# Kernel optimization log

Measured on AMD Instinct MI355X. Metric: run time of the kernel, lower is better.

Reference implementation:

```python
import jax, jax.numpy as jnp
from jax import lax
import numpy as np

B, CIN, CP, H, W = 16, 64, 64, 64, 64
K1 = 3   # deformable kernel
K2 = 5   # parallel conv kernel
EPS = 1e-5


def conv2d(x, w, stride, pad):
    return lax.conv_general_dilated(
        x, w, (stride, stride), [(pad, pad), (pad, pad)],
        dimension_numbers=('NCHW', 'OIHW', 'NCHW'))


def batchnorm(x, g, b, m, v):
    scale = g / jnp.sqrt(v + EPS)
    return (x - m[None, :, None, None]) * scale[None, :, None, None] + b[None, :, None, None]


def deform_conv2d(x, offset, weight, stride, pad):
    # x: [B,Cin,H,W], offset: [B,2*K*K,Ho,Wo] (dy,dx interleaved per kernel tap, torchvision layout)
    Bn, Cin, Hn, Wn = x.shape
    Cout, _, K, _ = weight.shape
    KK = K * K
    Ho, Wo = offset.shape[2], offset.shape[3]
    off = offset.reshape(Bn, KK, 2, Ho, Wo)
    dy, dx = off[:, :, 0], off[:, :, 1]                      # [B,KK,Ho,Wo]
    ky, kx = jnp.meshgrid(jnp.arange(K), jnp.arange(K), indexing='ij')
    ky = ky.reshape(KK).astype(x.dtype)
    kx = kx.reshape(KK).astype(x.dtype)
    base_y = (jnp.arange(Ho) * stride - pad).astype(x.dtype)
    base_x = (jnp.arange(Wo) * stride - pad).astype(x.dtype)
    ys = base_y[None, None, :, None] + ky[None, :, None, None] + dy  # [B,KK,Ho,Wo]
    xs = base_x[None, None, None, :] + kx[None, :, None, None] + dx
    y0 = jnp.floor(ys); x0 = jnp.floor(xs)
    wy1 = ys - y0; wx1 = xs - x0
    wy0 = 1.0 - wy1; wx0 = 1.0 - wx1
    flat = x.reshape(Bn, Cin, Hn * Wn)

    def gather(yi, xi):
        valid = ((yi >= 0) & (yi <= Hn - 1) & (xi >= 0) & (xi <= Wn - 1))
        yc = jnp.clip(yi, 0, Hn - 1).astype(jnp.int32)
        xc = jnp.clip(xi, 0, Wn - 1).astype(jnp.int32)
        idx = (yc * Wn + xc).reshape(Bn, -1)                 # [B,KK*Ho*Wo]
        g = jax.vmap(lambda f, i: jnp.take(f, i, axis=1))(flat, idx)
        g = g.reshape(Bn, Cin, KK, Ho, Wo)
        return g * valid.astype(x.dtype)[:, None]

    val = (gather(y0, x0) * (wy0 * wx0)[:, None]
           + gather(y0, x0 + 1) * (wy0 * wx1)[:, None]
           + gather(y0 + 1, x0) * (wy1 * wx0)[:, None]
           + gather(y0 + 1, x0 + 1) * (wy1 * wx1)[:, None])   # [B,Cin,KK,Ho,Wo]
    w_r = weight.reshape(Cout, Cin, KK)
    return jnp.einsum('bcknm,ock->bonm', val, w_r)


def setup_inputs():
    key = jax.random.key(0)
    ks = jax.random.split(key, 18)
    f32 = jnp.float32
    x = jax.random.normal(ks[0], (B, CIN, H, W), f32)
    w_off = jax.random.normal(ks[1], (2 * K1 * K1, CIN, 3, 3), f32) * 0.01
    b_off = jnp.zeros((2 * K1 * K1,), f32)
    w1 = jax.random.normal(ks[2], (CP, CIN, K1, K1), f32) / np.sqrt(CIN * K1 * K1)
    w3 = jax.random.normal(ks[3], (CP, CIN, K2, K2), f32) / np.sqrt(CIN * K2 * K2)
    w2 = jax.random.normal(ks[4], (CP, CP, 3, 3), f32) / np.sqrt(CP * 9)
    def bn(i):
        g = jax.random.uniform(ks[5 + 4 * i], (CP,), f32, 0.5, 1.5)
        b = jax.random.normal(ks[6 + 4 * i], (CP,), f32) * 0.1
        m = jax.random.normal(ks[7 + 4 * i], (CP,), f32) * 0.1
        v = jax.random.uniform(ks[8 + 4 * i], (CP,), f32, 0.5, 1.5)
        return g, b, m, v
    g1, b1, m1, v1 = bn(0)
    g3, b3, m3, v3 = bn(1)
    g2, b2, m2, v2 = bn(2)
    return dict(x=x, w_off=w_off, b_off=b_off, w1=w1, g1=g1, b1=b1, m1=m1, v1=v1,
                w3=w3, g3=g3, b3=b3, m3=m3, v3=v3, w2=w2, g2=g2, b2=b2, m2=m2, v2=v2)


def reference(x, w_off, b_off, w1, g1, b1, m1, v1, w3, g3, b3, m3, v3, w2, g2, b2, m2, v2):
    offset1 = conv2d(x, w_off, 1, 1) + b_off[None, :, None, None]
    out = jax.nn.relu(batchnorm(deform_conv2d(x, offset1, w1, 1, 1), g1, b1, m1, v1))
    out_1 = jax.nn.relu(batchnorm(conv2d(x, w3, 1, 2), g3, b3, m3, v3))
    out = out + out_1
    out = batchnorm(conv2d(out, w2, 1, 1), g2, b2, m2, v2)
    out = out + x  # identity shortcut (stride=1, in_planes==planes)
    return jax.nn.relu(out)
```

## Files before the change

kernel.cpp:

```cpp
#include <hip/hip_runtime.h>
#include <hip/hip_bf16.h>


#define HWv 4096
#define EPSv 1e-5f

typedef __attribute__((ext_vector_type(8))) short bf16x8;
typedef __attribute__((ext_vector_type(16))) float f32x16;
typedef __attribute__((ext_vector_type(2))) float f32x2;

__device__ inline ushort f2bf(float f) {
  __hip_bfloat16 h = __float2bfloat16(f);
  return *(ushort*)&h;
}
__device__ inline float bf2f(ushort u) {
  unsigned int t = ((unsigned int)u) << 16;
  union { unsigned int i; float f; } c; c.i = t; return c.f;
}
__device__ inline float bitsf(unsigned int u) {
  union { unsigned int i; float f; } c; c.i = u; return c.f;
}

__global__ __launch_bounds__(256) void prep_kernel(
    const float* __restrict__ x, const float* __restrict__ w3,
    const float* __restrict__ w2, const float* __restrict__ w1,
    const float* __restrict__ w_off,
    ushort* __restrict__ xT, ushort* __restrict__ w3F,
    ushort* __restrict__ w2F, ushort* __restrict__ w1F,
    ushort* __restrict__ wofF) {
  __shared__ float tile[64][65];
  const int blk = blockIdx.x;
  if (blk < 1024) {
    const int y = blk & 63, b = blk >> 6;
    for (int i = threadIdx.x; i < 4096; i += 256) {
      int ci = i >> 6, xx = i & 63;
      tile[ci][xx] = x[(((size_t)b * 64 + ci) * 64 + y) * 64 + xx];
    }
    __syncthreads();
    for (int i = threadIdx.x; i < 2048; i += 256) {
      int xx = i >> 5, cip = (i & 31) * 2;
      ushort2 v;
      v.x = f2bf(tile[cip][xx]);
      v.y = f2bf(tile[cip + 1][xx]);
      *(ushort2*)&xT[(((size_t)b * 64 + y) * 64 + xx) * 64 + cip] = v;
    }
    return;
  }
  int idx = (blk - 1024) * 256 + threadIdx.x;
  if (idx < 102400) {
    int j = idx & 7, lane = (idx >> 3) & 63, ks = (idx >> 9) & 3;
    int half = (idx >> 11) & 1, kk = idx >> 12;
    int ln = lane & 31, kh = lane >> 5;
    int co = half * 32 + ln, ci = ks * 16 + kh * 8 + j;
    w3F[idx] = f2bf(w3[(co * 64 + ci) * 25 + kk]);
    return;
  }
  idx -= 102400;
  if (idx < 36864) {
    int j = idx & 7, lane = (idx >> 3) & 63, ks = (idx >> 9) & 3;
    int half = (idx >> 11) & 1, kk = idx >> 12;
    int ln = lane & 31, kh = lane >> 5;
    int co = half * 32 + ln, ci = ks * 16 + kh * 8 + j;
    w2F[idx] = f2bf(w2[(co * 64 + ci) * 9 + kk]);
    return;
  }
  idx -= 36864;
  if (idx < 36864) {
    int j = idx & 7, lane = (idx >> 3) & 63, ks = (idx >> 9) & 3;
    int half = (idx >> 11) & 1, kk = idx >> 12;
    int ln = lane & 31, kh = lane >> 5;
    int co = half * 32 + ln, ci = ks * 16 + kh * 8 + j;
    w1F[idx] = f2bf(w1[(co * 64 + ci) * 9 + kk]);
    return;
  }
  idx -= 36864;
  if (idx < 18432) {
    int j = idx & 7, lane = (idx >> 3) & 63, ks = (idx >> 9) & 3;
    int kk = idx >> 11;
    int ln = lane & 31, kh = lane >> 5;
    int ci = ks * 16 + kh * 8 + j;
    wofF[idx] = f2bf(ln < 18 ? w_off[(ln * 64 + ci) * 9 + kk] : 0.f);
  }
}

__device__ __forceinline__ bf16x8 blend4(bf16x8 va, bf16x8 vb, bf16x8 vc, bf16x8 vd,
                                         f32x2 w00v, f32x2 w01v, f32x2 w10v, f32x2 w11v) {
  const unsigned int* ua = (const unsigned int*)&va;
  const unsigned int* ub = (const unsigned int*)&vb;
  const unsigned int* uc = (const unsigned int*)&vc;
  const unsigned int* ud = (const unsigned int*)&vd;
  bf16x8 f;
  ushort2* fo = (ushort2*)&f;
#pragma unroll
  for (int d = 0; d < 4; ++d) {
    f32x2 av = {bitsf(ua[d] << 16), bitsf(ua[d] & 0xFFFF0000u)};
    f32x2 bv = {bitsf(ub[d] << 16), bitsf(ub[d] & 0xFFFF0000u)};
    f32x2 cv = {bitsf(uc[d] << 16), bitsf(uc[d] & 0xFFFF0000u)};
    f32x2 dv = {bitsf(ud[d] << 16), bitsf(ud[d] & 0xFFFF0000u)};
    f32x2 r = w00v * av + w01v * bv + w10v * cv + w11v * dv;
    __hip_bfloat162 h2 = __float22bfloat162_rn(make_float2(r.x, r.y));
    fo[d] = *(ushort2*)&h2;
  }
  return f;
}

__global__ __launch_bounds__(256, 2) void fused_kernel(
    const ushort* __restrict__ xT, const ushort* __restrict__ wofF,
    const float* __restrict__ b_off, const ushort* __restrict__ w1F,
    const ushort* __restrict__ w3F,
    const float* __restrict__ g1, const float* __restrict__ b1,
    const float* __restrict__ m1, const float* __restrict__ v1,
    const float* __restrict__ g3, const float* __restrict__ b3,
    const float* __restrict__ m3, const float* __restrict__ v3,
    ushort* __restrict__ s1T) {
  __shared__ __align__(16) uint4 ldsx[6 * 68 * 8];
  __shared__ float stash[2 * 64 * 18];
  __shared__ float bn1s[64], bn1b[64], bn3s[64], bn3b[64];

  const int tid = threadIdx.x;
  const int wv = tid >> 6, lane = tid & 63;
  const int ln = lane & 31, kh = lane >> 5;
  const int r = wv >> 1, nt = wv & 1;
  const int y0 = blockIdx.x * 2, b = blockIdx.y;
  const int y = y0 + r, px = nt * 32 + ln;
  const uint4* xT4 = (const uint4*)xT;
  const bool interior = (y0 >= 2 && y0 <= 60);

  if (tid < 64) {
    float s = g1[tid] * rsqrtf(v1[tid] + EPSv);
    bn1s[tid] = s; bn1b[tid] = b1[tid] - m1[tid] * s;
    float s3 = g3[tid] * rsqrtf(v3[tid] + EPSv);
    bn3s[tid] = s3; bn3b[tid] = b3[tid] - m3[tid] * s3;
  }
  for (int i = tid; i < 6 * 68 * 8; i += 256) {
    int tr = i / (68 * 8), rem = i % (68 * 8);
    int col = rem >> 3, c = rem & 7;
    int ysrc = min(max(y0 - 2 + tr, 0), 63);
    int xcol = col - 2;
    uint4 v = make_uint4(0, 0, 0, 0);
    if (xcol >= 0 && xcol <= 63)
      v = xT4[((size_t)((b * 64 + ysrc) * 64 + xcol)) * 8 + c];
    ldsx[(tr * 68 + col) * 8 + (c ^ (col & 7))] = v;
  }
  __syncthreads();

  f32x16 acco;
#pragma unroll
  for (int j = 0; j < 16; ++j) acco[j] = 0.f;
  if (interior) {
#pragma unroll
    for (int kk = 0; kk < 9; ++kk) {
      const int ky = kk / 3, kx = kk % 3;
      const int tr = r + ky + 1;
      const int col = px + kx + 1;
      bf16x8 af[4], bf[4];
#pragma unroll
      for (int ks = 0; ks < 4; ++ks)
        af[ks] = *(const bf16x8*)&wofF[(size_t)((kk * 4 + ks) * 64 + lane) * 8];
#pragma unroll
      for (int ks = 0; ks < 4; ++ks) {
        int c = ks * 2 + kh;
        bf[ks] = *(const bf16x8*)&ldsx[(tr * 68 + col) * 8 + (c ^ (col & 7))];
      }
#pragma unroll
      for (int ks = 0; ks < 4; ++ks)
        acco = __builtin_amdgcn_mfma_f32_32x32x16_bf16(af[ks], bf[ks], acco, 0, 0, 0);
    }
  } else {
#pragma unroll
    for (int kk = 0; kk < 9; ++kk) {
      const int ky = kk / 3, kx = kk % 3;
      const int yy = y - 1 + ky;
      if (yy >= 0 && yy <= 63) {
        const int tr = yy - (y0 - 2);
        const int col = px + kx + 1;
#pragma unroll
        for (int ks = 0; ks < 4; ++ks) {
          int c = ks * 2 + kh;
          bf16x8 af = *(const bf16x8*)&wofF[(size_t)((kk * 4 + ks) * 64 + lane) * 8];
          bf16x8 bf = *(const bf16x8*)&ldsx[(tr * 68 + col) * 8 + (c ^ (col & 7))];
          acco = __builtin_amdgcn_mfma_f32_32x32x16_bf16(af, bf, acco, 0, 0, 0);
        }
      }
    }
  }
#pragma unroll
  for (int reg = 0; reg < 16; ++reg) {
    int co = (reg & 3) + 8 * (reg >> 2) + 4 * kh;
    if (co < 18)
      stash[(r * 64 + px) * 18 + co] = acco[reg] + b_off[co];
  }
  __syncthreads();

  float dyv[9], dxv[9];
#pragma unroll
  for (int kk = 0; kk < 9; ++kk) {
    dyv[kk] = stash[(r * 64 + px) * 18 + 2 * kk];
    dxv[kk] = stash[(r * 64 + px) * 18 + 2 * kk + 1];
  }
  bool fast = true;
#pragma unroll
  for (int kk = 0; kk < 9; ++kk) {
    int iy0 = (int)floorf((float)(y - 1 + kk / 3) + dyv[kk]);
    int iy1 = iy0 + 1;
    bool ok0 = (iy0 < 0) || (iy0 > 63) || (iy0 >= y0 - 2 && iy0 <= y0 + 3);
    bool ok1 = (iy1 < 0) || (iy1 > 63) || (iy1 >= y0 - 2 && iy1 <= y0 + 3);
    fast = fast && ok0 && ok1;
  }

  f32x16 accd0, accd1;
#pragma unroll
  for (int j = 0; j < 16; ++j) { accd0[j] = 0.f; accd1[j] = 0.f; }
  const ushort* xb = xT + (size_t)b * 64 * 64 * 64;

  if (__ballot(!fast) == 0ull) {
#pragma unroll
    for (int kk = 0; kk < 9; ++kk) {
      const int ky = kk / 3, kx = kk % 3;
      float ys = (float)(y - 1 + ky) + dyv[kk];
      float xs = (float)(px - 1 + kx) + dxv[kk];
      float y0f = floorf(ys), x0f = floorf(xs);
      float wy1 = ys - y0f, wx1 = xs - x0f;
      float wy0 = 1.f - wy1, wx0 = 1.f - wx1;
      int iy0 = (int)y0f, ix0 = (int)x0f;
      int iy1 = iy0 + 1, ix1 = ix0 + 1;
      float vy0 = (iy0 >= 0 && iy0 <= 63) ? 1.f : 0.f;
      float vy1 = (iy1 >= 0 && iy1 <= 63) ? 1.f : 0.f;
      float vx0 = (ix0 >= 0 && ix0 <= 63) ? 1.f : 0.f;
      float vx1 = (ix1 >= 0 && ix1 <= 63) ? 1.f : 0.f;
      int x0c = min(max(ix0, 0), 63), x1c = min(max(ix1, 0), 63);
      float w00 = wy0 * wx0 * vy0 * vx0;
      float w01 = wy0 * wx1 * vy0 * vx1;
      float w10 = wy1 * wx0 * vy1 * vx0;
      float w11 = wy1 * wx1 * vy1 * vx1;
      int tr0 = min(max(iy0 - (y0 - 2), 0), 5);
      int tr1 = min(max(iy1 - (y0 - 2), 0), 5);
      int c0 = x0c + 2, c1 = x1c + 2;
      f32x2 w00v = {w00, w00}, w01v = {w01, w01};
      f32x2 w10v = {w10, w10}, w11v = {w11, w11};

      bf16x8 a0[4], a1[4], va[4], vb[4], vc[4], vd[4];
#pragma unroll
      for (int ks = 0; ks < 4; ++ks) {
        a0[ks] = *(const bf16x8*)&w1F[(size_t)(((kk * 2 + 0) * 4 + ks) * 64 + lane) * 8];
        a1[ks] = *(const bf16x8*)&w1F[(size_t)(((kk * 2 + 1) * 4 + ks) * 64 + lane) * 8];
      }
#pragma unroll
      for (int ks = 0; ks < 4; ++ks) {
        int c = ks * 2 + kh;
        va[ks] = *(const bf16x8*)&ldsx[(tr0 * 68 + c0) * 8 + (c ^ (c0 & 7))];
        vb[ks] = *(const bf16x8*)&ldsx[(tr0 * 68 + c1) * 8 + (c ^ (c1 & 7))];
        vc[ks] = *(const bf16x8*)&ldsx[(tr1 * 68 + c0) * 8 + (c ^ (c0 & 7))];
        vd[ks] = *(const bf16x8*)&ldsx[(tr1 * 68 + c1) * 8 + (c ^ (c1 & 7))];
      }
#pragma unroll
      for (int ks = 0; ks < 4; ++ks) {
        bf16x8 f = blend4(va[ks], vb[ks], vc[ks], vd[ks], w00v, w01v, w10v, w11v);
        accd0 = __builtin_amdgcn_mfma_f32_32x32x16_bf16(a0[ks], f, accd0, 0, 0, 0);
        accd1 = __builtin_amdgcn_mfma_f32_32x32x16_bf16(a1[ks], f, accd1, 0, 0, 0);
      }
    }
  } else {
#pragma unroll
    for (int kk = 0; kk < 9; ++kk) {
      const int ky = kk / 3, kx = kk % 3;
      float ys = (float)(y - 1 + ky) + dyv[kk];
      float xs = (float)(px - 1 + kx) + dxv[kk];
      float y0f = floorf(ys), x0f = floorf(xs);
      float wy1 = ys - y0f, wx1 = xs - x0f;
      float wy0 = 1.f - wy1, wx0 = 1.f - wx1;
      int iy0 = (int)y0f, ix0 = (int)x0f;
      int iy1 = iy0 + 1, ix1 = ix0 + 1;
      float vy0 = (iy0 >= 0 && iy0 <= 63) ? 1.f : 0.f;
      float vy1 = (iy1 >= 0 && iy1 <= 63) ? 1.f : 0.f;
      float vx0 = (ix0 >= 0 && ix0 <= 63) ? 1.f : 0.f;
      float vx1 = (ix1 >= 0 && ix1 <= 63) ? 1.f : 0.f;
      int x0c = min(max(ix0, 0), 63), x1c = min(max(ix1, 0), 63);
      float w00 = wy0 * wx0 * vy0 * vx0;
      float w01 = wy0 * wx1 * vy0 * vx1;
      float w10 = wy1 * wx0 * vy1 * vx0;
      float w11 = wy1 * wx1 * vy1 * vx1;
      int tr0 = min(max(iy0 - (y0 - 2), 0), 5);
      int tr1 = min(max(iy1 - (y0 - 2), 0), 5);
      int c0 = x0c + 2, c1 = x1c + 2;
      f32x2 w00v = {w00, w00}, w01v = {w01, w01};
      f32x2 w10v = {w10, w10}, w11v = {w11, w11};

      bf16x8 frag[4];
#pragma unroll
      for (int ks = 0; ks < 4; ++ks) {
        int c = ks * 2 + kh;
        bf16x8 va = *(const bf16x8*)&ldsx[(tr0 * 68 + c0) * 8 + (c ^ (c0 & 7))];
        bf16x8 vb = *(const bf16x8*)&ldsx[(tr0 * 68 + c1) * 8 + (c ^ (c1 & 7))];
        bf16x8 vc = *(const bf16x8*)&ldsx[(tr1 * 68 + c0) * 8 + (c ^ (c0 & 7))];
        bf16x8 vd = *(const bf16x8*)&ldsx[(tr1 * 68 + c1) * 8 + (c ^ (c1 & 7))];
        frag[ks] = blend4(va, vb, vc, vd, w00v, w01v, w10v, w11v);
      }
      if (!fast) {
        int y0c = min(max(iy0, 0), 63), y1c = min(max(iy1, 0), 63);
        const ushort* p00 = xb + (y0c * 64 + x0c) * 64 + kh * 8;
        const ushort* p01 = xb + (y0c * 64 + x1c) * 64 + kh * 8;
        const ushort* p10 = xb + (y1c * 64 + x0c) * 64 + kh * 8;
        const ushort* p11 = xb + (y1c * 64 + x1c) * 64 + kh * 8;
#pragma unroll
        for (int ks = 0; ks < 4; ++ks) {
          bf16x8 va = *(const bf16x8*)(p00 + ks * 16);
          bf16x8 vb = *(const bf16x8*)(p01 + ks * 16);
          bf16x8 vc = *(const bf16x8*)(p10 + ks * 16);
          bf16x8 vd = *(const bf16x8*)(p11 + ks * 16);
          frag[ks] = blend4(va, vb, vc, vd, w00v, w01v, w10v, w11v);
        }
      }
#pragma unroll
      for (int ks = 0; ks < 4; ++ks) {
        bf16x8 a0 = *(const bf16x8*)&w1F[(size_t)(((kk * 2 + 0) * 4 + ks) * 64 + lane) * 8];
        bf16x8 a1 = *(const bf16x8*)&w1F[(size_t)(((kk * 2 + 1) * 4 + ks) * 64 + lane) * 8];
        accd0 = __builtin_amdgcn_mfma_f32_32x32x16_bf16(a0, frag[ks], accd0, 0, 0, 0);
        accd1 = __builtin_amdgcn_mfma_f32_32x32x16_bf16(a1, frag[ks], accd1, 0, 0, 0);
      }
    }
  }

  f32x16 acc50, acc51;
#pragma unroll
  for (int j = 0; j < 16; ++j) { acc50[j] = 0.f; acc51[j] = 0.f; }
  if (interior) {
#pragma unroll
    for (int kk = 0; kk < 25; ++kk) {
      const int ky = kk / 5, kx = kk % 5;
      const int tr = r + ky;
      const int col = px + kx;
      bf16x8 a0[4], a1[4], bfv[4];
#pragma unroll
      for (int ks = 0; ks < 4; ++ks) {
        a0[ks] = *(const bf16x8*)&w3F[(size_t)(((kk * 2 + 0) * 4 + ks) * 64 + lane) * 8];
        a1[ks] = *(const bf16x8*)&w3F[(size_t)(((kk * 2 + 1) * 4 + ks) * 64 + lane) * 8];
      }
#pragma unroll
      for (int ks = 0; ks < 4; ++ks) {
        int c = ks * 2 + kh;
        bfv[ks] = *(const bf16x8*)&ldsx[(tr * 68 + col) * 8 + (c ^ (col & 7))];
      }
#pragma unroll
      for (int ks = 0; ks < 4; ++ks) {
        acc50 = __builtin_amdgcn_mfma_f32_32x32x16_bf16(a0[ks], bfv[ks], acc50, 0, 0, 0);
        acc51 = __builtin_amdgcn_mfma_f32_32x32x16_bf16(a1[ks], bfv[ks], acc51, 0, 0, 0);
      }
    }
  } else {
#pragma unroll
    for (int kk = 0; kk < 25; ++kk) {
      const int ky = kk / 5, kx = kk % 5;
      const int yy = y - 2 + ky;
      if (yy >= 0 && yy <= 63) {
        const int tr = r + ky;
        const int col = px + kx;
#pragma unroll
        for (int ks = 0; ks < 4; ++ks) {
          int c = ks * 2 + kh;
          bf16x8 bf = *(const bf16x8*)&ldsx[(tr * 68 + col) * 8 + (c ^ (col & 7))];
          bf16x8 a0 = *(const bf16x8*)&w3F[(size_t)(((kk * 2 + 0) * 4 + ks) * 64 + lane) * 8];
          bf16x8 a1 = *(const bf16x8*)&w3F[(size_t)(((kk * 2 + 1) * 4 + ks) * 64 + lane) * 8];
          acc50 = __builtin_amdgcn_mfma_f32_32x32x16_bf16(a0, bf, acc50, 0, 0, 0);
          acc51 = __builtin_amdgcn_mfma_f32_32x32x16_bf16(a1, bf, acc51, 0, 0, 0);
        }
      }
    }
  }

  ushort* op = s1T + ((size_t)((b * 64 + y) * 64 + px)) * 64;
#pragma unroll
  for (int q = 0; q < 4; ++q) {
    int co0 = 8 * q + 4 * kh;
    float vv[4];
#pragma unroll
    for (int rr = 0; rr < 4; ++rr) {
      int co = co0 + rr;
      float vd = accd0[q * 4 + rr] * bn1s[co] + bn1b[co];
      vd = vd > 0.f ? vd : 0.f;
      float v5 = acc50[q * 4 + rr] * bn3s[co] + bn3b[co];
      v5 = v5 > 0.f ? v5 : 0.f;
      vv[rr] = vd + v5;
    }
    ushort4 st;
    st.x = f2bf(vv[0]); st.y = f2bf(vv[1]); st.z = f2bf(vv[2]); st.w = f2bf(vv[3]);
    *(ushort4*)(op + co0) = st;
#pragma unroll
    for (int rr = 0; rr < 4; ++rr) {
      int co = co0 + 32 + rr;
      float vd = accd1[q * 4 + rr] * bn1s[co] + bn1b[co];
      vd = vd > 0.f ? vd : 0.f;
      float v5 = acc51[q * 4 + rr] * bn3s[co] + bn3b[co];
      v5 = v5 > 0.f ? v5 : 0.f;
      vv[rr] = vd + v5;
    }
    st.x = f2bf(vv[0]); st.y = f2bf(vv[1]); st.z = f2bf(vv[2]); st.w = f2bf(vv[3]);
    *(ushort4*)(op + co0 + 32) = st;
  }
}

__global__ __launch_bounds__(256, 2) void conv3_mfma_kernel(
    const ushort* __restrict__ s1T, const ushort* __restrict__ w2F,
    const float* __restrict__ g2, const float* __restrict__ b2,
    const float* __restrict__ m2, const float* __restrict__ v2,
    const float* __restrict__ x, float* __restrict__ out) {
  __shared__ __align__(16) uint4 Bt[3 * 66 * 8];
  __shared__ float sc[64], bi[64];
  const int tid = threadIdx.x;
  if (tid < 64) {
    float s = g2[tid] * rsqrtf(v2[tid] + EPSv);
    sc[tid] = s;
    bi[tid] = b2[tid] - m2[tid] * s;
  }
  const int y = blockIdx.x, b = blockIdx.y;
  const int wv = tid >> 6, lane = tid & 63;
  const int ln = lane & 31, kh = lane >> 5;
  const int mh = wv & 1, nt = wv >> 1;
  const int px = nt * 32 + ln;
  const uint4* s1T4 = (const uint4*)s1T;

  for (int i = tid; i < 3 * 66 * 8; i += 256) {
    int tr = i / (66 * 8), rem = i % (66 * 8);
    int col = rem >> 3, c = rem & 7;
    int yy = y - 1 + tr, xcol = col - 1;
    uint4 v = make_uint4(0, 0, 0, 0);
    if (yy >= 0 && yy <= 63 && xcol >= 0 && xcol <= 63)
      v = s1T4[((size_t)((b * 64 + yy) * 64 + xcol)) * 8 + c];
    Bt[(tr * 66 + col) * 8 + (c ^ (col & 7))] = v;
  }
  __syncthreads();

  f32x16 acc;
#pragma unroll
  for (int j = 0; j < 16; ++j) acc[j] = 0.f;

#pragma unroll
  for (int kk = 0; kk < 9; ++kk) {
    const int ky = kk / 3, kx = kk % 3;
    const int col = px + kx;
    bf16x8 af[4], bfr[4];
#pragma unroll
    for (int ccb = 0; ccb < 4; ++ccb)
      af[ccb] = *(const bf16x8*)&w2F[(size_t)(((kk * 2 + mh) * 4 + ccb) * 64 + lane) * 8];
#pragma unroll
    for (int ccb = 0; ccb < 4; ++ccb) {
      int c = ccb * 2 + kh;
      bfr[ccb] = *(const bf16x8*)&Bt[(ky * 66 + col) * 8 + (c ^ (col & 7))];
    }
#pragma unroll
    for (int ccb = 0; ccb < 4; ++ccb)
      acc = __builtin_amdgcn_mfma_f32_32x32x16_bf16(af[ccb], bfr[ccb], acc, 0, 0, 0);
  }
#pragma unroll
  for (int reg = 0; reg < 16; ++reg) {
    int co = (reg & 3) + 8 * (reg >> 2) + 4 * kh + mh * 32;
    size_t o = (((size_t)b * 64 + co) * 64 + y) * 64 + px;
    float v = acc[reg] * sc[co] + bi[co] + x[o];
    out[o] = v > 0.f ? v : 0.f;
  }
}

extern "C" void kernel_launch(void* const* d_in, const int* in_sizes, int n_in,
                              void* d_out, int out_size, void* d_ws, size_t ws_size,
                              hipStream_t stream) {
  const float* x     = (const float*)d_in[0];
  const float* w_off = (const float*)d_in[1];
  const float* b_off = (const float*)d_in[2];
  const float* w1    = (const float*)d_in[3];
  const float* g1    = (const float*)d_in[4];
  const float* b1    = (const float*)d_in[5];
  const float* m1    = (const float*)d_in[6];
  const float* v1    = (const float*)d_in[7];
  const float* w3    = (const float*)d_in[8];
  const float* g3    = (const float*)d_in[9];
  const float* b3    = (const float*)d_in[10];
  const float* m3    = (const float*)d_in[11];
  const float* v3    = (const float*)d_in[12];
  const float* w2    = (const float*)d_in[13];
  const float* g2    = (const float*)d_in[14];
  const float* b2    = (const float*)d_in[15];
  const float* m2    = (const float*)d_in[16];
  const float* v2    = (const float*)d_in[17];
  float* out = (float*)d_out;

  ushort* xT   = (ushort*)d_ws;
  ushort* s1T  = xT + (size_t)16 * 64 * HWv;
  ushort* w3F  = s1T + (size_t)16 * 64 * HWv;
  ushort* w2F  = w3F + 102400;
  ushort* w1F  = w2F + 36864;
  ushort* wofF = w1F + 36864;

  prep_kernel<<<dim3(1024 + 760), dim3(256), 0, stream>>>(x, w3, w2, w1, w_off,
                                                          xT, w3F, w2F, w1F, wofF);
  fused_kernel<<<dim3(32, 16), dim3(256), 0, stream>>>(xT, wofF, b_off, w1F, w3F,
                                                       g1, b1, m1, v1, g3, b3, m3, v3,
                                                       s1T);
  conv3_mfma_kernel<<<dim3(64, 16), dim3(256), 0, stream>>>(s1T, w2F, g2, b2, m2, v2,
                                                            x, out);
}
```

Baseline: 69.00 us.

## Split fused kernel K-dimension across two wave halves with LDS reduction

Doubles the fused kernel's block to 512 threads and splits each MFMA reduction over input channels into two halves, one per wave group. Partial offset-conv results are summed through two LDS stash buffers, and the deform and 5x5 accumulators are reduced through a swizzled LDS exchange before the BN/ReLU epilogue. The aim is more waves per CU to hide LDS and gather latency, since the grid has only 512 blocks. The cost is extra barriers, LDS traffic for the reductions, a larger LDS footprint, and half the waves idling during the epilogue.

```diff
diff --git a/kernel.cpp b/kernel.cpp
--- a/kernel.cpp
+++ b/kernel.cpp
@@ -104,7 +104,7 @@
   return f;
 }
 
-__global__ __launch_bounds__(256, 2) void fused_kernel(
+__global__ __launch_bounds__(512, 4) void fused_kernel(
     const ushort* __restrict__ xT, const ushort* __restrict__ wofF,
     const float* __restrict__ b_off, const ushort* __restrict__ w1F,
     const ushort* __restrict__ w3F,
@@ -113,14 +113,18 @@
     const float* __restrict__ g3, const float* __restrict__ b3,
     const float* __restrict__ m3, const float* __restrict__ v3,
     ushort* __restrict__ s1T) {
-  __shared__ __align__(16) uint4 ldsx[6 * 68 * 8];
-  __shared__ float stash[2 * 64 * 18];
-  __shared__ float bn1s[64], bn1b[64], bn3s[64], bn3b[64];
+  __shared__ __align__(16) unsigned char smem[71680];
+  uint4* ldsx = (uint4*)smem;
+  float* stash = (float*)(smem + 52224);
+  float* bn1s = (float*)(smem + 70656);
+  float* bn1b = bn1s + 64;
+  float* bn3s = bn1s + 128;
+  float* bn3b = bn1s + 192;
 
   const int tid = threadIdx.x;
   const int wv = tid >> 6, lane = tid & 63;
   const int ln = lane & 31, kh = lane >> 5;
-  const int r = wv >> 1, nt = wv & 1;
+  const int ksh = wv & 1, nt = (wv >> 1) & 1, r = wv >> 2;
   const int y0 = blockIdx.x * 2, b = blockIdx.y;
   const int y = y0 + r, px = nt * 32 + ln;
   const uint4* xT4 = (const uint4*)xT;
@@ -132,7 +136,7 @@
     float s3 = g3[tid] * rsqrtf(v3[tid] + EPSv);
     bn3s[tid] = s3; bn3b[tid] = b3[tid] - m3[tid] * s3;
   }
-  for (int i = tid; i < 6 * 68 * 8; i += 256) {
+  for (int i = tid; i < 6 * 68 * 8; i += 512) {
     int tr = i / (68 * 8), rem = i % (68 * 8);
     int col = rem >> 3, c = rem & 7;
     int ysrc = min(max(y0 - 2 + tr, 0), 63);
@@ -153,18 +157,20 @@
       const int ky = kk / 3, kx = kk % 3;
       const int tr = r + ky + 1;
       const int col = px + kx + 1;
-      bf16x8 af[4], bf[4];
-#pragma unroll
-      for (int ks = 0; ks < 4; ++ks)
-        af[ks] = *(const bf16x8*)&wofF[(size_t)((kk * 4 + ks) * 64 + lane) * 8];
-#pragma unroll
-      for (int ks = 0; ks < 4; ++ks) {
-        int c = ks * 2 + kh;
-        bf[ks] = *(const bf16x8*)&ldsx[(tr * 68 + col) * 8 + (c ^ (col & 7))];
-      }
-#pragma unroll
-      for (int ks = 0; ks < 4; ++ks)
-        acco = __builtin_amdgcn_mfma_f32_32x32x16_bf16(af[ks], bf[ks], acco, 0, 0, 0);
+      bf16x8 af[2], bfv[2];
+#pragma unroll
+      for (int ksq = 0; ksq < 2; ++ksq) {
+        int ks = ksh * 2 + ksq;
+        af[ksq] = *(const bf16x8*)&wofF[(size_t)((kk * 4 + ks) * 64 + lane) * 8];
+      }
+#pragma unroll
+      for (int ksq = 0; ksq < 2; ++ksq) {
+        int c = (ksh * 2 + ksq) * 2 + kh;
+        bfv[ksq] = *(const bf16x8*)&ldsx[(tr * 68 + col) * 8 + (c ^ (col & 7))];
+      }
+#pragma unroll
+      for (int ksq = 0; ksq < 2; ++ksq)
+        acco = __builtin_amdgcn_mfma_f32_32x32x16_bf16(af[ksq], bfv[ksq], acco, 0, 0, 0);
     }
   } else {
 #pragma unroll
@@ -175,7 +181,8 @@
         const int tr = yy - (y0 - 2);
         const int col = px + kx + 1;
 #pragma unroll
-        for (int ks = 0; ks < 4; ++ks) {
+        for (int ksq = 0; ksq < 2; ++ksq) {
+          int ks = ksh * 2 + ksq;
           int c = ks * 2 + kh;
           bf16x8 af = *(const bf16x8*)&wofF[(size_t)((kk * 4 + ks) * 64 + lane) * 8];
           bf16x8 bf = *(const bf16x8*)&ldsx[(tr * 68 + col) * 8 + (c ^ (col & 7))];
@@ -184,19 +191,23 @@
       }
     }
   }
-#pragma unroll
-  for (int reg = 0; reg < 16; ++reg) {
-    int co = (reg & 3) + 8 * (reg >> 2) + 4 * kh;
-    if (co < 18)
-      stash[(r * 64 + px) * 18 + co] = acco[reg] + b_off[co];
+  {
+    float* stb = stash + ksh * 2304;
+#pragma unroll
+    for (int reg = 0; reg < 16; ++reg) {
+      int co = (reg & 3) + 8 * (reg >> 2) + 4 * kh;
+      if (co < 18)
+        stb[(r * 64 + px) * 18 + co] = acco[reg] + (ksh ? 0.f : b_off[co]);
+    }
   }
   __syncthreads();
 
   float dyv[9], dxv[9];
+  const int sb = (r * 64 + px) * 18;
 #pragma unroll
   for (int kk = 0; kk < 9; ++kk) {
-    dyv[kk] = stash[(r * 64 + px) * 18 + 2 * kk];
-    dxv[kk] = stash[(r * 64 + px) * 18 + 2 * kk + 1];
+    dyv[kk] = stash[sb + 2 * kk] + stash[2304 + sb + 2 * kk];
+    dxv[kk] = stash[sb + 2 * kk + 1] + stash[2304 + sb + 2 * kk + 1];
   }
   bool fast = true;
 #pragma unroll
@@ -239,25 +250,26 @@
       f32x2 w00v = {w00, w00}, w01v = {w01, w01};
       f32x2 w10v = {w10, w10}, w11v = {w11, w11};
 
-      bf16x8 a0[4], a1[4], va[4], vb[4], vc[4], vd[4];
-#pragma unroll
-      for (int ks = 0; ks < 4; ++ks) {
-        a0[ks] = *(const bf16x8*)&w1F[(size_t)(((kk * 2 + 0) * 4 + ks) * 64 + lane) * 8];
-        a1[ks] = *(const bf16x8*)&w1F[(size_t)(((kk * 2 + 1) * 4 + ks) * 64 + lane) * 8];
-      }
-#pragma unroll
-      for (int ks = 0; ks < 4; ++ks) {
-        int c = ks * 2 + kh;
-        va[ks] = *(const bf16x8*)&ldsx[(tr0 * 68 + c0) * 8 + (c ^ (c0 & 7))];
-        vb[ks] = *(const bf16x8*)&ldsx[(tr0 * 68 + c1) * 8 + (c ^ (c1 & 7))];
-        vc[ks] = *(const bf16x8*)&ldsx[(tr1 * 68 + c0) * 8 + (c ^ (c0 & 7))];
-        vd[ks] = *(const bf16x8*)&ldsx[(tr1 * 68 + c1) * 8 + (c ^ (c1 & 7))];
-      }
-#pragma unroll
-      for (int ks = 0; ks < 4; ++ks) {
-        bf16x8 f = blend4(va[ks], vb[ks], vc[ks], vd[ks], w00v, w01v, w10v, w11v);
-        accd0 = __builtin_amdgcn_mfma_f32_32x32x16_bf16(a0[ks], f, accd0, 0, 0, 0);
-        accd1 = __builtin_amdgcn_mfma_f32_32x32x16_bf16(a1[ks], f, accd1, 0, 0, 0);
+      bf16x8 a0[2], a1[2], va[2], vb[2], vc[2], vd[2];
+#pragma unroll
+      for (int ksq = 0; ksq < 2; ++ksq) {
+        int ks = ksh * 2 + ksq;
+        a0[ksq] = *(const bf16x8*)&w1F[(size_t)(((kk * 2 + 0) * 4 + ks) * 64 + lane) * 8];
+        a1[ksq] = *(const bf16x8*)&w1F[(size_t)(((kk * 2 + 1) * 4 + ks) * 64 + lane) * 8];
+      }
+#pragma unroll
+      for (int ksq = 0; ksq < 2; ++ksq) {
+        int c = (ksh * 2 + ksq) * 2 + kh;
+        va[ksq] = *(const bf16x8*)&ldsx[(tr0 * 68 + c0) * 8 + (c ^ (c0 & 7))];
+        vb[ksq] = *(const bf16x8*)&ldsx[(tr0 * 68 + c1) * 8 + (c ^ (c1 & 7))];
+        vc[ksq] = *(const bf16x8*)&ldsx[(tr1 * 68 + c0) * 8 + (c ^ (c0 & 7))];
+        vd[ksq] = *(const bf16x8*)&ldsx[(tr1 * 68 + c1) * 8 + (c ^ (c1 & 7))];
+      }
+#pragma unroll
+      for (int ksq = 0; ksq < 2; ++ksq) {
+        bf16x8 f = blend4(va[ksq], vb[ksq], vc[ksq], vd[ksq], w00v, w01v, w10v, w11v);
+        accd0 = __builtin_amdgcn_mfma_f32_32x32x16_bf16(a0[ksq], f, accd0, 0, 0, 0);
+        accd1 = __builtin_amdgcn_mfma_f32_32x32x16_bf16(a1[ksq], f, accd1, 0, 0, 0);
       }
     }
   } else {
@@ -286,15 +298,15 @@
       f32x2 w00v = {w00, w00}, w01v = {w01, w01};
       f32x2 w10v = {w10, w10}, w11v = {w11, w11};
 
-      bf16x8 frag[4];
-#pragma unroll
-      for (int ks = 0; ks < 4; ++ks) {
-        int c = ks * 2 + kh;
+      bf16x8 frag[2];
+#pragma unroll
+      for (int ksq = 0; ksq < 2; ++ksq) {
+        int c = (ksh * 2 + ksq) * 2 + kh;
         bf16x8 va = *(const bf16x8*)&ldsx[(tr0 * 68 + c0) * 8 + (c ^ (c0 & 7))];
         bf16x8 vb = *(const bf16x8*)&ldsx[(tr0 * 68 + c1) * 8 + (c ^ (c1 & 7))];
         bf16x8 vc = *(const bf16x8*)&ldsx[(tr1 * 68 + c0) * 8 + (c ^ (c0 & 7))];
         bf16x8 vd = *(const bf16x8*)&ldsx[(tr1 * 68 + c1) * 8 + (c ^ (c1 & 7))];
-        frag[ks] = blend4(va, vb, vc, vd, w00v, w01v, w10v, w11v);
+        frag[ksq] = blend4(va, vb, vc, vd, w00v, w01v, w10v, w11v);
       }
       if (!fast) {
         int y0c = min(max(iy0, 0), 63), y1c = min(max(iy1, 0), 63);
@@ -303,20 +315,22 @@
         const ushort* p10 = xb + (y1c * 64 + x0c) * 64 + kh * 8;
         const ushort* p11 = xb + (y1c * 64 + x1c) * 64 + kh * 8;
 #pragma unroll
-        for (int ks = 0; ks < 4; ++ks) {
+        for (int ksq = 0; ksq < 2; ++ksq) {
+          int ks = ksh * 2 + ksq;
           bf16x8 va = *(const bf16x8*)(p00 + ks * 16);
           bf16x8 vb = *(const bf16x8*)(p01 + ks * 16);
           bf16x8 vc = *(const bf16x8*)(p10 + ks * 16);
           bf16x8 vd = *(const bf16x8*)(p11 + ks * 16);
-          frag[ks] = blend4(va, vb, vc, vd, w00v, w01v, w10v, w11v);
+          frag[ksq] = blend4(va, vb, vc, vd, w00v, w01v, w10v, w11v);
         }
       }
 #pragma unroll
-      for (int ks = 0; ks < 4; ++ks) {
+      for (int ksq = 0; ksq < 2; ++ksq) {
+        int ks = ksh * 2 + ksq;
         bf16x8 a0 = *(const bf16x8*)&w1F[(size_t)(((kk * 2 + 0) * 4 + ks) * 64 + lane) * 8];
         bf16x8 a1 = *(const bf16x8*)&w1F[(size_t)(((kk * 2 + 1) * 4 + ks) * 64 + lane) * 8];
-        accd0 = __builtin_amdgcn_mfma_f32_32x32x16_bf16(a0, frag[ks], accd0, 0, 0, 0);
-        accd1 = __builtin_amdgcn_mfma_f32_32x32x16_bf16(a1, frag[ks], accd1, 0, 0, 0);
+        accd0 = __builtin_amdgcn_mfma_f32_32x32x16_bf16(a0, frag[ksq], accd0, 0, 0, 0);
+        accd1 = __builtin_amdgcn_mfma_f32_32x32x16_bf16(a1, frag[ksq], accd1, 0, 0, 0);
       }
     }
   }
@@ -330,21 +344,22 @@
       const int ky = kk / 5, kx = kk % 5;
       const int tr = r + ky;
       const int col = px + kx;
-      bf16x8 a0[4], a1[4], bfv[4];
-#pragma unroll
-      for (int ks = 0; ks < 4; ++ks) {
-        a0[ks] = *(const bf16x8*)&w3F[(size_t)(((kk * 2 + 0) * 4 + ks) * 64 + lane) * 8];
-        a1[ks] = *(const bf16x8*)&w3F[(size_t)(((kk * 2 + 1) * 4 + ks) * 64 + lane) * 8];
-      }
-#pragma unroll
-      for (int ks = 0; ks < 4; ++ks) {
-        int c = ks * 2 + kh;
-        bfv[ks] = *(const bf16x8*)&ldsx[(tr * 68 + col) * 8 + (c ^ (col & 7))];
-      }
-#pragma unroll
-      for (int ks = 0; ks < 4; ++ks) {
-        acc50 = __builtin_amdgcn_mfma_f32_32x32x16_bf16(a0[ks], bfv[ks], acc50, 0, 0, 0);
-        acc51 = __builtin_amdgcn_mfma_f32_32x32x16_bf16(a1[ks], bfv[ks], acc51, 0, 0, 0);
+      bf16x8 a0[2], a1[2], bfv[2];
+#pragma unroll
+      for (int ksq = 0; ksq < 2; ++ksq) {
+        int ks = ksh * 2 + ksq;
+        a0[ksq] = *(const bf16x8*)&w3F[(size_t)(((kk * 2 + 0) * 4 + ks) * 64 + lane) * 8];
+        a1[ksq] = *(const bf16x8*)&w3F[(size_t)(((kk * 2 + 1) * 4 + ks) * 64 + lane) * 8];
+      }
+#pragma unroll
+      for (int ksq = 0; ksq < 2; ++ksq) {
+        int c = (ksh * 2 + ksq) * 2 + kh;
+        bfv[ksq] = *(const bf16x8*)&ldsx[(tr * 68 + col) * 8 + (c ^ (col & 7))];
+      }
+#pragma unroll
+      for (int ksq = 0; ksq < 2; ++ksq) {
+        acc50 = __builtin_amdgcn_mfma_f32_32x32x16_bf16(a0[ksq], bfv[ksq], acc50, 0, 0, 0);
+        acc51 = __builtin_amdgcn_mfma_f32_32x32x16_bf16(a1[ksq], bfv[ksq], acc51, 0, 0, 0);
       }
     }
   } else {
@@ -356,7 +371,8 @@
         const int tr = r + ky;
         const int col = px + kx;
 #pragma unroll
-        for (int ks = 0; ks < 4; ++ks) {
+        for (int ksq = 0; ksq < 2; ++ksq) {
+          int ks = ksh * 2 + ksq;
           int c = ks * 2 + kh;
           bf16x8 bf = *(const bf16x8*)&ldsx[(tr * 68 + col) * 8 + (c ^ (col & 7))];
           bf16x8 a0 = *(const bf16x8*)&w3F[(size_t)(((kk * 2 + 0) * 4 + ks) * 64 + lane) * 8];
@@ -368,34 +384,75 @@
     }
   }
 
-  ushort* op = s1T + ((size_t)((b * 64 + y) * 64 + px)) * 64;
-#pragma unroll
-  for (int q = 0; q < 4; ++q) {
-    int co0 = 8 * q + 4 * kh;
-    float vv[4];
-#pragma unroll
-    for (int rr = 0; rr < 4; ++rr) {
-      int co = co0 + rr;
-      float vd = accd0[q * 4 + rr] * bn1s[co] + bn1b[co];
-      vd = vd > 0.f ? vd : 0.f;
-      float v5 = acc50[q * 4 + rr] * bn3s[co] + bn3b[co];
-      v5 = v5 > 0.f ? v5 : 0.f;
-      vv[rr] = vd + v5;
-    }
-    ushort4 st;
-    st.x = f2bf(vv[0]); st.y = f2bf(vv[1]); st.z = f2bf(vv[2]); st.w = f2bf(vv[3]);
-    *(ushort4*)(op + co0) = st;
-#pragma unroll
-    for (int rr = 0; rr < 4; ++rr) {
-      int co = co0 + 32 + rr;
-      float vd = accd1[q * 4 + rr] * bn1s[co] + bn1b[co];
-      vd = vd > 0.f ? vd : 0.f;
-      float v5 = acc51[q * 4 + rr] * bn3s[co] + bn3b[co];
-      v5 = v5 > 0.f ? v5 : 0.f;
-      vv[rr] = vd + v5;
-    }
-    st.x = f2bf(vv[0]); st.y = f2bf(vv[1]); st.z = f2bf(vv[2]); st.w = f2bf(vv[3]);
-    *(ushort4*)(op + co0 + 32) = st;
+  __syncthreads();
+  float4* sp = (float4*)((float*)smem + ((size_t)((r * 2 + nt) * 64 + lane)) * 32);
+  const int sw = lane & 7;
+  if (ksh) {
+    union { f32x16 v; float4 q[4]; } ua, ub;
+    ua.v = accd0; ub.v = accd1;
+    sp[0 ^ sw] = ua.q[0]; sp[1 ^ sw] = ua.q[1];
+    sp[2 ^ sw] = ua.q[2]; sp[3 ^ sw] = ua.q[3];
+    sp[4 ^ sw] = ub.q[0]; sp[5 ^ sw] = ub.q[1];
+    sp[6 ^ sw] = ub.q[2]; sp[7 ^ sw] = ub.q[3];
+  }
+  __syncthreads();
+  if (!ksh) {
+    union { f32x16 v; float4 q[4]; } ua, ub;
+    ua.q[0] = sp[0 ^ sw]; ua.q[1] = sp[1 ^ sw];
+    ua.q[2] = sp[2 ^ sw]; ua.q[3] = sp[3 ^ sw];
+    ub.q[0] = sp[4 ^ sw]; ub.q[1] = sp[5 ^ sw];
+    ub.q[2] = sp[6 ^ sw]; ub.q[3] = sp[7 ^ sw];
+    accd0 = accd0 + ua.v;
+    accd1 = accd1 + ub.v;
+  }
+  __syncthreads();
+  if (ksh) {
+    union { f32x16 v; float4 q[4]; } ua, ub;
+    ua.v = acc50; ub.v = acc51;
+    sp[0 ^ sw] = ua.q[0]; sp[1 ^ sw] = ua.q[1];
+    sp[2 ^ sw] = ua.q[2]; sp[3 ^ sw] = ua.q[3];
+    sp[4 ^ sw] = ub.q[0]; sp[5 ^ sw] = ub.q[1];
+    sp[6 ^ sw] = ub.q[2]; sp[7 ^ sw] = ub.q[3];
+  }
+  __syncthreads();
+  if (!ksh) {
+    union { f32x16 v; float4 q[4]; } ua, ub;
+    ua.q[0] = sp[0 ^ sw]; ua.q[1] = sp[1 ^ sw];
+    ua.q[2] = sp[2 ^ sw]; ua.q[3] = sp[3 ^ sw];
+    ub.q[0] = sp[4 ^ sw]; ub.q[1] = sp[5 ^ sw];
+    ub.q[2] = sp[6 ^ sw]; ub.q[3] = sp[7 ^ sw];
+    acc50 = acc50 + ua.v;
+    acc51 = acc51 + ub.v;
+
+    ushort* op = s1T + ((size_t)((b * 64 + y) * 64 + px)) * 64;
+#pragma unroll
+    for (int q = 0; q < 4; ++q) {
+      int co0 = 8 * q + 4 * kh;
+      float vv[4];
+#pragma unroll
+      for (int rr = 0; rr < 4; ++rr) {
+        int co = co0 + rr;
+        float vd = accd0[q * 4 + rr] * bn1s[co] + bn1b[co];
+        vd = vd > 0.f ? vd : 0.f;
+        float v5 = acc50[q * 4 + rr] * bn3s[co] + bn3b[co];
+        v5 = v5 > 0.f ? v5 : 0.f;
+        vv[rr] = vd + v5;
+      }
+      ushort4 st;
+      st.x = f2bf(vv[0]); st.y = f2bf(vv[1]); st.z = f2bf(vv[2]); st.w = f2bf(vv[3]);
+      *(ushort4*)(op + co0) = st;
+#pragma unroll
+      for (int rr = 0; rr < 4; ++rr) {
+        int co = co0 + 32 + rr;
+        float vd = accd1[q * 4 + rr] * bn1s[co] + bn1b[co];
+        vd = vd > 0.f ? vd : 0.f;
+        float v5 = acc51[q * 4 + rr] * bn3s[co] + bn3b[co];
+        v5 = v5 > 0.f ? v5 : 0.f;
+        vv[rr] = vd + v5;
+      }
+      st.x = f2bf(vv[0]); st.y = f2bf(vv[1]); st.z = f2bf(vv[2]); st.w = f2bf(vv[3]);
+      *(ushort4*)(op + co0 + 32) = st;
+    }
   }
 }
 
@@ -492,7 +549,7 @@
 
   prep_kernel<<<dim3(1024 + 760), dim3(256), 0, stream>>>(x, w3, w2, w1, w_off,
                                                           xT, w3F, w2F, w1F, wofF);
-  fused_kernel<<<dim3(32, 16), dim3(256), 0, stream>>>(xT, wofF, b_off, w1F, w3F,
+  fused_kernel<<<dim3(32, 16), dim3(512), 0, stream>>>(xT, wofF, b_off, w1F, w3F,
                                                        g1, b1, m1, v1, g3, b3, m3, v3,
                                                        s1T);
   conv3_mfma_kernel<<<dim3(64, 16), dim3(256), 0, stream>>>(s1T, w2F, g2, b2, m2, v2,
```

Result: no change. 70.07 us (+1.6%).
